# Performance work log

Hardware: AMD Instinct MI355X
Metric: run time of the kernel (lower is better)

## Reference

```python
import jax, jax.numpy as jnp
import numpy as np

B, C, W, H, D = 2, 256, 32, 32, 32
CH = C // 2  # 128
LN_EPS = 1e-5


def _spatial_pool(x, wm, bm):
    # x: [B,C,W,H,D]; wm: [C]; bm: scalar. 1x1x1 conv C->1 == channel dot.
    b, c = x.shape[0], x.shape[1]
    xf = x.reshape(b, c, -1)                       # [B,C,N]
    mask = jnp.einsum('bcn,c->bn', xf, wm) + bm    # [B,N]
    attn = jax.nn.softmax(mask, axis=1)            # softmax over spatial N
    return jnp.einsum('bcn,bn->bc', xf, attn)      # [B,C] weighted-sum pool


def _channel_add(ctx, w1, b1, g, be, w2, b2):
    # 1x1 conv C->C/2, LayerNorm over C/2, ReLU, 1x1 conv C/2->C
    h = ctx @ w1.T + b1                            # [B,CH]
    mu = jnp.mean(h, axis=-1, keepdims=True)
    var = jnp.mean((h - mu) ** 2, axis=-1, keepdims=True)
    h = (h - mu) * jax.lax.rsqrt(var + LN_EPS) * g + be
    h = jax.nn.relu(h)
    return h @ w2.T + b2                           # [B,C]


def setup_inputs() -> dict:
    key = jax.random.key(0)
    ks = jax.random.split(key, 20)
    s = 0.02
    d = {
        'preds_S': jax.random.normal(ks[0], (B, C, W, H, D), jnp.float32),
        'preds_T': jax.random.normal(ks[1], (B, C, W, H, D), jnp.float32),
        'wm_s': jax.random.normal(ks[2], (C,), jnp.float32) * s,
        'bm_s': jnp.zeros((), jnp.float32),
        'wm_t': jax.random.normal(ks[3], (C,), jnp.float32) * s,
        'bm_t': jnp.zeros((), jnp.float32),
        'w1_s': jax.random.normal(ks[4], (CH, C), jnp.float32) * s,
        'b1_s': jnp.zeros((CH,), jnp.float32),
        'g_s': jnp.ones((CH,), jnp.float32),
        'be_s': jnp.zeros((CH,), jnp.float32),
        'w2_s': jax.random.normal(ks[5], (C, CH), jnp.float32) * s,
        'b2_s': jnp.zeros((C,), jnp.float32),
        'w1_t': jax.random.normal(ks[6], (CH, C), jnp.float32) * s,
        'b1_t': jnp.zeros((CH,), jnp.float32),
        'g_t': jnp.ones((CH,), jnp.float32),
        'be_t': jnp.zeros((CH,), jnp.float32),
        'w2_t': jax.random.normal(ks[7], (C, CH), jnp.float32) * s,
        'b2_t': jnp.zeros((C,), jnp.float32),
    }
    return d


def reference(preds_S, preds_T, wm_s, bm_s, wm_t, bm_t,
              w1_s, b1_s, g_s, be_s, w2_s, b2_s,
              w1_t, b1_t, g_t, be_t, w2_t, b2_t):
    ctx_s = _spatial_pool(preds_S, wm_s, bm_s)     # [B,C]
    ctx_t = _spatial_pool(preds_T, wm_t, bm_t)
    add_s = _channel_add(ctx_s, w1_s, b1_s, g_s, be_s, w2_s, b2_s)  # [B,C]
    add_t = _channel_add(ctx_t, w1_t, b1_t, g_t, be_t, w2_t, b2_t)
    out_s = preds_S + add_s[:, :, None, None, None]
    out_t = preds_T + add_t[:, :, None, None, None]
    diff = out_s - out_t
    return jnp.sum(diff * diff) / preds_S.shape[0]
```

## Files before the change

### kernel.cpp

```cpp
#include <hip/hip_runtime.h>
#include <math.h>

#define Bc   2
#define Cc   256
#define Nn   32768
#define CHc  128
#define LN_EPS 1e-5f

#define TN    64
#define TPB   512
#define NQ    16
#define CG    32
#define CPG   8
#define GRIDX (Nn / TN)

__global__ __launch_bounds__(TPB) void gc_fused(
    const float* __restrict__ S, const float* __restrict__ T,
    const float* __restrict__ wms, const float* __restrict__ bms,
    const float* __restrict__ wmt, const float* __restrict__ bmt,
    float* __restrict__ ctxnum,
    float* __restrict__ rowsum,
    float* __restrict__ den,
    float* __restrict__ sumsq) {
  const int b    = blockIdx.y;
  const int tid  = threadIdx.x;
  const int nq   = tid & (NQ - 1);
  const int cg   = tid >> 4;
  const int wv   = tid >> 6;
  const int lane = tid & 63;
  const int c0   = cg * CPG;
  const int n0   = blockIdx.x * TN + nq * 4;

  __shared__ float4 mredw[2][8][NQ];
  __shared__ float  credA[Cc * 17];
  __shared__ float  credB[Cc * 17];
  __shared__ float  credC[Cc * 17];
  __shared__ float  sqred[8];
  __shared__ float  denred[2][NQ];

  const float bS = bms[0];
  const float bT = bmt[0];

  const float* Sp = S + ((size_t)b * Cc + c0) * Nn + n0;
  const float* Tp = T + ((size_t)b * Cc + c0) * Nn + n0;

  float4 s4[CPG], t4[CPG];
#pragma unroll
  for (int i = 0; i < CPG; ++i) s4[i] = *(const float4*)(Sp + (size_t)i * Nn);
#pragma unroll
  for (int i = 0; i < CPG; ++i) t4[i] = *(const float4*)(Tp + (size_t)i * Nn);

  float wS[CPG], wT[CPG];
#pragma unroll
  for (int i = 0; i < CPG; ++i) { wS[i] = wms[c0 + i]; wT[i] = wmt[c0 + i]; }

  float4 ms = make_float4(0.f, 0.f, 0.f, 0.f);
  float4 mt = make_float4(0.f, 0.f, 0.f, 0.f);
  float rs[CPG];
  float sq = 0.f;
#pragma unroll
  for (int i = 0; i < CPG; ++i) {
    ms.x += wS[i] * s4[i].x; ms.y += wS[i] * s4[i].y;
    ms.z += wS[i] * s4[i].z; ms.w += wS[i] * s4[i].w;
    mt.x += wT[i] * t4[i].x; mt.y += wT[i] * t4[i].y;
    mt.z += wT[i] * t4[i].z; mt.w += wT[i] * t4[i].w;
    const float dx = s4[i].x - t4[i].x, dy = s4[i].y - t4[i].y;
    const float dz = s4[i].z - t4[i].z, dw = s4[i].w - t4[i].w;
    rs[i] = dx + dy + dz + dw;
    sq += dx * dx + dy * dy + dz * dz + dw * dw;
  }

#pragma unroll
  for (int m = 16; m <= 32; m <<= 1) {
    ms.x += __shfl_xor(ms.x, m); ms.y += __shfl_xor(ms.y, m);
    ms.z += __shfl_xor(ms.z, m); ms.w += __shfl_xor(ms.w, m);
    mt.x += __shfl_xor(mt.x, m); mt.y += __shfl_xor(mt.y, m);
    mt.z += __shfl_xor(mt.z, m); mt.w += __shfl_xor(mt.w, m);
  }
  if (lane < NQ) { mredw[0][wv][nq] = ms; mredw[1][wv][nq] = mt; }

#pragma unroll
  for (int m = 1; m < 64; m <<= 1) sq += __shfl_xor(sq, m);
  if (lane == 0) sqred[wv] = sq;

  __syncthreads();

  float4 Ms = make_float4(0.f, 0.f, 0.f, 0.f);
  float4 Mt = make_float4(0.f, 0.f, 0.f, 0.f);
#pragma unroll
  for (int w = 0; w < 8; ++w) {
    const float4 a = mredw[0][w][nq];
    Ms.x += a.x; Ms.y += a.y; Ms.z += a.z; Ms.w += a.w;
    const float4 c = mredw[1][w][nq];
    Mt.x += c.x; Mt.y += c.y; Mt.z += c.z; Mt.w += c.w;
  }
  float4 es, et;
  es.x = __expf(Ms.x + bS); es.y = __expf(Ms.y + bS);
  es.z = __expf(Ms.z + bS); es.w = __expf(Ms.w + bS);
  et.x = __expf(Mt.x + bT); et.y = __expf(Mt.y + bT);
  et.z = __expf(Mt.z + bT); et.w = __expf(Mt.w + bT);

  if (tid < NQ) {
    denred[0][tid] = es.x + es.y + es.z + es.w;
    denred[1][tid] = et.x + et.y + et.z + et.w;
  }

#pragma unroll
  for (int i = 0; i < CPG; ++i) {
    credA[(c0 + i) * 17 + nq] =
        s4[i].x * es.x + s4[i].y * es.y + s4[i].z * es.z + s4[i].w * es.w;
    credB[(c0 + i) * 17 + nq] =
        t4[i].x * et.x + t4[i].y * et.y + t4[i].z * et.z + t4[i].w * et.w;
    credC[(c0 + i) * 17 + nq] = rs[i];
  }
  __syncthreads();

  if (tid < Cc) {
    float a = 0.f, c = 0.f, r = 0.f;
#pragma unroll
    for (int k = 0; k < NQ; ++k) {
      a += credA[tid * 17 + k];
      c += credB[tid * 17 + k];
      r += credC[tid * 17 + k];
    }
    atomicAdd(&ctxnum[((size_t)0 * Bc + b) * Cc + tid], a);
    atomicAdd(&ctxnum[((size_t)1 * Bc + b) * Cc + tid], c);
    atomicAdd(&rowsum[(size_t)b * Cc + tid], r);
  } else if (tid == Cc) {
    float v = 0.f;
#pragma unroll
    for (int w = 0; w < 8; ++w) v += sqred[w];
    atomicAdd(sumsq, v);
  } else if (tid == Cc + 1) {
    float a = 0.f, c = 0.f;
#pragma unroll
    for (int k = 0; k < NQ; ++k) { a += denred[0][k]; c += denred[1][k]; }
    atomicAdd(&den[0 * Bc + b], a);
    atomicAdd(&den[1 * Bc + b], c);
  }
}

__global__ __launch_bounds__(1024) void gc_k4a_mlp(
    const float* __restrict__ ctxr, const float* __restrict__ den,
    const float* __restrict__ w1s, const float* __restrict__ b1s,
    const float* __restrict__ gs,  const float* __restrict__ bes,
    const float* __restrict__ w2s, const float* __restrict__ b2s,
    const float* __restrict__ w1t, const float* __restrict__ b1t,
    const float* __restrict__ gt,  const float* __restrict__ bet,
    const float* __restrict__ w2t, const float* __restrict__ b2t,
    float* __restrict__ addv) {
  const int tt  = blockIdx.x >> 1;
  const int b   = blockIdx.x & 1;
  const int tid = threadIdx.x;

  const float* w1 = tt ? w1t : w1s;
  const float* b1 = tt ? b1t : b1s;
  const float* g  = tt ? gt  : gs;
  const float* be = tt ? bet : bes;
  const float* w2 = tt ? w2t : w2s;
  const float* b2 = tt ? b2t : b2s;

  __shared__ float cxs[Cc];
  __shared__ float part[1024];
  __shared__ float hbuf[CHc];
  __shared__ float hr[CHc];
  __shared__ float2 red2[128];
  __shared__ float mu_s, rstd_s;

  if (tid < Cc)
    cxs[tid] = ctxr[((size_t)tt * Bc + b) * Cc + tid] / den[tt * Bc + b];
  __syncthreads();

  {
    const int j = tid >> 3, s = tid & 7;
    const float* wr = w1 + j * Cc + s * 32;
    const float4* cx4 = (const float4*)(cxs + s * 32);
    float acc = 0.f;
#pragma unroll
    for (int k = 0; k < 8; ++k) {
      const float4 w = *(const float4*)(wr + k * 4);
      const float4 x = cx4[k];
      acc += w.x * x.x + w.y * x.y + w.z * x.z + w.w * x.w;
    }
    part[tid] = acc;
  }
  __syncthreads();
  if (tid < CHc) {
    float h = b1[tid];
#pragma unroll
    for (int q = 0; q < 8; ++q) h += part[tid * 8 + q];
    hbuf[tid] = h;
  }
  __syncthreads();

  if (tid < CHc) {
    const float v = hbuf[tid];
    red2[tid] = make_float2(v, v * v);
  }
  __syncthreads();
  for (int s = 64; s > 0; s >>= 1) {
    if (tid < s) {
      red2[tid].x += red2[tid + s].x;
      red2[tid].y += red2[tid + s].y;
    }
    __syncthreads();
  }
  if (tid == 0) {
    const float mu = red2[0].x / (float)CHc;
    const float var = red2[0].y / (float)CHc - mu * mu;
    mu_s = mu;
    rstd_s = rsqrtf(var + LN_EPS);
  }
  __syncthreads();
  if (tid < CHc) {
    const float v = (hbuf[tid] - mu_s) * rstd_s * g[tid] + be[tid];
    hr[tid] = v > 0.f ? v : 0.f;
  }
  __syncthreads();

  {
    const int c = tid >> 2, q = tid & 3;
    const float* wr = w2 + c * CHc + q * 32;
    const float4* h4 = (const float4*)(hr + q * 32);
    float acc = 0.f;
#pragma unroll
    for (int k = 0; k < 8; ++k) {
      const float4 w = *(const float4*)(wr + k * 4);
      const float4 x = h4[k];
      acc += w.x * x.x + w.y * x.y + w.z * x.z + w.w * x.w;
    }
    part[tid] = acc;
  }
  __syncthreads();
  if (tid < Cc) {
    float acc = b2[tid];
#pragma unroll
    for (int q = 0; q < 4; ++q) acc += part[tid * 4 + q];
    addv[((size_t)tt * Bc + b) * Cc + tid] = acc;
  }
}

__global__ __launch_bounds__(256) void gc_k4b_final(
    const float* __restrict__ addv, const float* __restrict__ rowsum,
    const float* __restrict__ sumsq, float* __restrict__ out) {
  const int tid = threadIdx.x;
  __shared__ float red[256];
  float part = 0.f;
  for (int job = tid; job < Bc * Cc; job += 256) {
    const int c = job & (Cc - 1);
    const int b = job >> 8;
    const float delta = addv[((size_t)0 * Bc + b) * Cc + c] -
                        addv[((size_t)1 * Bc + b) * Cc + c];
    part += 2.f * delta * rowsum[(size_t)b * Cc + c] +
            (float)Nn * delta * delta;
  }
  red[tid] = part;
  __syncthreads();
  for (int s = 128; s > 0; s >>= 1) {
    if (tid < s) red[tid] += red[tid + s];
    __syncthreads();
  }
  if (tid == 0) out[0] = (red[0] + sumsq[0]) / (float)Bc;
}

extern "C" void kernel_launch(void* const* d_in, const int* in_sizes, int n_in,
                              void* d_out, int out_size, void* d_ws,
                              size_t ws_size, hipStream_t stream) {
  const float* S   = (const float*)d_in[0];
  const float* T   = (const float*)d_in[1];
  const float* wms = (const float*)d_in[2];
  const float* bms = (const float*)d_in[3];
  const float* wmt = (const float*)d_in[4];
  const float* bmt = (const float*)d_in[5];
  const float* w1s = (const float*)d_in[6];
  const float* b1s = (const float*)d_in[7];
  const float* gs  = (const float*)d_in[8];
  const float* bes = (const float*)d_in[9];
  const float* w2s = (const float*)d_in[10];
  const float* b2s = (const float*)d_in[11];
  const float* w1t = (const float*)d_in[12];
  const float* b1t = (const float*)d_in[13];
  const float* gt  = (const float*)d_in[14];
  const float* bet = (const float*)d_in[15];
  const float* w2t = (const float*)d_in[16];
  const float* b2t = (const float*)d_in[17];
  float* out = (float*)d_out;

  float* ws     = (float*)d_ws;
  float* ctxnum = ws;
  float* rowsum = ctxnum + 2 * Bc * Cc;
  float* den    = rowsum + Bc * Cc;
  float* sumsq  = den + 4;
  float* addv   = sumsq + 1;

  hipMemsetAsync(d_ws, 0, (2 * Bc * Cc + Bc * Cc + 4 + 1) * sizeof(float),
                 stream);

  gc_fused<<<dim3(GRIDX, Bc), TPB, 0, stream>>>(S, T, wms, bms, wmt, bmt,
                                                ctxnum, rowsum, den, sumsq);
  gc_k4a_mlp<<<4, 1024, 0, stream>>>(ctxnum, den, w1s, b1s, gs, bes, w2s, b2s,
                                     w1t, b1t, gt, bet, w2t, b2t, addv);
  gc_k4b_final<<<1, 256, 0, stream>>>(addv, rowsum, sumsq, out);
}
```

Before: 208.4 us.

## Reuse one shared reduction buffer across three phases and request two blocks per CU

```diff
diff --git a/kernel.cpp b/kernel.cpp
--- a/kernel.cpp
+++ b/kernel.cpp
@@ -14,7 +14,7 @@
 #define CPG   8
 #define GRIDX (Nn / TN)
 
-__global__ __launch_bounds__(TPB) void gc_fused(
+__global__ __launch_bounds__(TPB, 2) void gc_fused(
     const float* __restrict__ S, const float* __restrict__ T,
     const float* __restrict__ wms, const float* __restrict__ bms,
     const float* __restrict__ wmt, const float* __restrict__ bmt,
@@ -32,9 +32,7 @@
   const int n0   = blockIdx.x * TN + nq * 4;
 
   __shared__ float4 mredw[2][8][NQ];
-  __shared__ float  credA[Cc * 17];
-  __shared__ float  credB[Cc * 17];
-  __shared__ float  credC[Cc * 17];
+  __shared__ float  cred[Cc * 17];
   __shared__ float  sqred[8];
   __shared__ float  denred[2][NQ];
 
@@ -56,18 +54,12 @@
 
   float4 ms = make_float4(0.f, 0.f, 0.f, 0.f);
   float4 mt = make_float4(0.f, 0.f, 0.f, 0.f);
-  float rs[CPG];
-  float sq = 0.f;
 #pragma unroll
   for (int i = 0; i < CPG; ++i) {
     ms.x += wS[i] * s4[i].x; ms.y += wS[i] * s4[i].y;
     ms.z += wS[i] * s4[i].z; ms.w += wS[i] * s4[i].w;
     mt.x += wT[i] * t4[i].x; mt.y += wT[i] * t4[i].y;
     mt.z += wT[i] * t4[i].z; mt.w += wT[i] * t4[i].w;
-    const float dx = s4[i].x - t4[i].x, dy = s4[i].y - t4[i].y;
-    const float dz = s4[i].z - t4[i].z, dw = s4[i].w - t4[i].w;
-    rs[i] = dx + dy + dz + dw;
-    sq += dx * dx + dy * dy + dz * dz + dw * dw;
   }
 
 #pragma unroll
@@ -79,10 +71,6 @@
   }
   if (lane < NQ) { mredw[0][wv][nq] = ms; mredw[1][wv][nq] = mt; }
 
-#pragma unroll
-  for (int m = 1; m < 64; m <<= 1) sq += __shfl_xor(sq, m);
-  if (lane == 0) sqred[wv] = sq;
-
   __syncthreads();
 
   float4 Ms = make_float4(0.f, 0.f, 0.f, 0.f);
@@ -106,37 +94,59 @@
   }
 
 #pragma unroll
+  for (int i = 0; i < CPG; ++i)
+    cred[(c0 + i) * 17 + nq] =
+        s4[i].x * es.x + s4[i].y * es.y + s4[i].z * es.z + s4[i].w * es.w;
+  __syncthreads();
+  if (tid < Cc) {
+    float a = 0.f;
+#pragma unroll
+    for (int k = 0; k < NQ; ++k) a += cred[tid * 17 + k];
+    atomicAdd(&ctxnum[((size_t)0 * Bc + b) * Cc + tid], a);
+  } else if (tid == Cc + 1) {
+    float a = 0.f, c = 0.f;
+#pragma unroll
+    for (int k = 0; k < NQ; ++k) { a += denred[0][k]; c += denred[1][k]; }
+    atomicAdd(&den[0 * Bc + b], a);
+    atomicAdd(&den[1 * Bc + b], c);
+  }
+  __syncthreads();
+
+#pragma unroll
+  for (int i = 0; i < CPG; ++i)
+    cred[(c0 + i) * 17 + nq] =
+        t4[i].x * et.x + t4[i].y * et.y + t4[i].z * et.z + t4[i].w * et.w;
+  __syncthreads();
+  if (tid < Cc) {
+    float c = 0.f;
+#pragma unroll
+    for (int k = 0; k < NQ; ++k) c += cred[tid * 17 + k];
+    atomicAdd(&ctxnum[((size_t)1 * Bc + b) * Cc + tid], c);
+  }
+  __syncthreads();
+
+  float sq = 0.f;
+#pragma unroll
   for (int i = 0; i < CPG; ++i) {
-    credA[(c0 + i) * 17 + nq] =
-        s4[i].x * es.x + s4[i].y * es.y + s4[i].z * es.z + s4[i].w * es.w;
-    credB[(c0 + i) * 17 + nq] =
-        t4[i].x * et.x + t4[i].y * et.y + t4[i].z * et.z + t4[i].w * et.w;
-    credC[(c0 + i) * 17 + nq] = rs[i];
-  }
-  __syncthreads();
-
+    const float dx = s4[i].x - t4[i].x, dy = s4[i].y - t4[i].y;
+    const float dz = s4[i].z - t4[i].z, dw = s4[i].w - t4[i].w;
+    cred[(c0 + i) * 17 + nq] = dx + dy + dz + dw;
+    sq += dx * dx + dy * dy + dz * dz + dw * dw;
+  }
+#pragma unroll
+  for (int m = 1; m < 64; m <<= 1) sq += __shfl_xor(sq, m);
+  if (lane == 0) sqred[wv] = sq;
+  __syncthreads();
   if (tid < Cc) {
-    float a = 0.f, c = 0.f, r = 0.f;
-#pragma unroll
-    for (int k = 0; k < NQ; ++k) {
-      a += credA[tid * 17 + k];
-      c += credB[tid * 17 + k];
-      r += credC[tid * 17 + k];
-    }
-    atomicAdd(&ctxnum[((size_t)0 * Bc + b) * Cc + tid], a);
-    atomicAdd(&ctxnum[((size_t)1 * Bc + b) * Cc + tid], c);
+    float r = 0.f;
+#pragma unroll
+    for (int k = 0; k < NQ; ++k) r += cred[tid * 17 + k];
     atomicAdd(&rowsum[(size_t)b * Cc + tid], r);
   } else if (tid == Cc) {
     float v = 0.f;
 #pragma unroll
     for (int w = 0; w < 8; ++w) v += sqred[w];
     atomicAdd(sumsq, v);
-  } else if (tid == Cc + 1) {
-    float a = 0.f, c = 0.f;
-#pragma unroll
-    for (int k = 0; k < NQ; ++k) { a += denred[0][k]; c += denred[1][k]; }
-    atomicAdd(&den[0 * Bc + b], a);
-    atomicAdd(&den[1 * Bc + b], c);
   }
 }
 
```

Result: no change. 207.9 us (-0.2%).
